# Optimization experiments

Hardware: AMD Instinct MI355X
Metric: run time of the kernel (lower is better)

Reference implementation:

```python
import jax, jax.numpy as jnp
import numpy as np

CODEBOOK_SIZE = 1024
EMBEDDING_DIM = 64


def setup_inputs() -> dict:
    key = jax.random.key(0)
    k_in, k_cb = jax.random.split(key)
    # latent feature (batch, embedding_dim, length)
    input = jax.random.normal(k_in, (16, EMBEDDING_DIM, 8192), dtype=jnp.float32)
    # learned codebook table (codebook_size, embedding_dim)
    codebook = jax.random.normal(k_cb, (CODEBOOK_SIZE, EMBEDDING_DIM), dtype=jnp.float32)
    return {"input": input, "codebook": codebook}


def reference(input, codebook):
    # input: (B, D, T); codebook: (K, D)
    B, D = input.shape[0], input.shape[1]
    spatial = input.shape[2:]
    # move embedding dim last and flatten tokens: (B*T, D)
    x = jnp.moveaxis(input, 1, -1).reshape(-1, D)
    x_sq = jnp.sum(x * x, axis=-1, keepdims=True)            # (N, 1)
    e_sq = jnp.sum(codebook * codebook, axis=-1)             # (K,)
    dist = x_sq - 2.0 * (x @ codebook.T) + e_sq[None, :]     # (N, K)
    indices = jnp.argmin(dist, axis=-1)                      # (N,)
    quantized = jnp.take(codebook, indices, axis=0)          # (N, D)
    # reshape back: output (B, D, *spatial), indices (B, *spatial)
    out = jnp.moveaxis(quantized.reshape((B,) + spatial + (D,)), -1, 1)
    idx = indices.reshape((B,) + spatial)
    return out, idx
```

## Files before the change

### kernel.cpp

```cpp
#include <hip/hip_runtime.h>
#include <float.h>

#define K_CODES 1024
#define DIM 64
#define T_LEN 8192
#define N_TOK 131072
#define LO_SCALE 2048.0f
#define LO_INV   (1.0f / 2048.0f)

typedef _Float16 half8 __attribute__((ext_vector_type(8)));
typedef float    f32x4 __attribute__((ext_vector_type(4)));

__global__ void vq_prep(const float* __restrict__ cb,
                        _Float16* __restrict__ whi,
                        _Float16* __restrict__ wlo,
                        float* __restrict__ wesq) {
    const int code = blockIdx.x * 256 + threadIdx.x;
    const float* row = cb + (size_t)code * DIM;
    float s = 0.0f;
    #pragma unroll
    for (int d0 = 0; d0 < DIM; d0 += 4) {
        float4 v = *reinterpret_cast<const float4*>(row + d0);
        float x[4] = {v.x, v.y, v.z, v.w};
        #pragma unroll
        for (int j = 0; j < 4; ++j) {
            float xx = x[j];
            _Float16 h = (_Float16)xx;
            _Float16 l = (_Float16)((xx - (float)h) * LO_SCALE);
            whi[(size_t)code * DIM + d0 + j] = h;
            wlo[(size_t)code * DIM + d0 + j] = l;
            s = fmaf(xx, xx, s);
        }
    }
    wesq[code] = s;
}

__global__ __launch_bounds__(256, 2)
void vq_main(const float* __restrict__ in,
             const float* __restrict__ cb,
             const _Float16* __restrict__ whi,
             const _Float16* __restrict__ wlo,
             const float* __restrict__ wesq,
             float* __restrict__ out) {
    __shared__ float esq_s[K_CODES];
    __shared__ int   idx_s[256];

    const int tid  = threadIdx.x;
    const int wave = tid >> 6;
    const int lane = tid & 63;
    const int lo4  = lane & 15;
    const int quad = lane >> 4;

    for (int k = tid; k < K_CODES; k += 256) esq_s[k] = wesq[k];
    __syncthreads();

    const int strip = (blockIdx.x * 4 + wave) * 64;
    const int b  = strip >> 13;
    const int t0 = strip & 8191;

    const float* xin = in + (size_t)b * DIM * T_LEN + t0;
    half8 a_hi[4][2], a_lo[4][2];
    #pragma unroll
    for (int mt = 0; mt < 4; ++mt) {
        #pragma unroll
        for (int s = 0; s < 2; ++s) {
            #pragma unroll
            for (int j = 0; j < 8; ++j) {
                const int d = s * 32 + quad * 8 + j;
                float x = xin[(size_t)d * T_LEN + mt * 16 + lo4];
                _Float16 h = (_Float16)x;
                _Float16 l = (_Float16)((x - (float)h) * LO_SCALE);
                a_hi[mt][s][j] = h;
                a_lo[mt][s][j] = l;
            }
        }
    }

    float best[16];
    int   bidx[16];
    #pragma unroll
    for (int i = 0; i < 16; ++i) { best[i] = FLT_MAX; bidx[i] = 0; }

    const _Float16* hbase = whi + (size_t)lo4 * DIM + quad * 8;
    const _Float16* lbase = wlo + (size_t)lo4 * DIM + quad * 8;

    half8 cbh0 = *(const half8*)(hbase);
    half8 cbh1 = *(const half8*)(hbase + 32);
    half8 cbl0 = *(const half8*)(lbase);
    half8 cbl1 = *(const half8*)(lbase + 32);
    float cesq = esq_s[lo4];

    for (int ct = 0; ct < 64; ++ct) {
        const int nct = (ct < 63) ? (ct + 1) : 63;
        const size_t noff = (size_t)nct * 16 * DIM;
        half8 nbh0 = *(const half8*)(hbase + noff);
        half8 nbh1 = *(const half8*)(hbase + noff + 32);
        half8 nbl0 = *(const half8*)(lbase + noff);
        half8 nbl1 = *(const half8*)(lbase + noff + 32);
        float nesq = esq_s[nct * 16 + lo4];

        const int code = ct * 16 + lo4;
        #pragma unroll
        for (int mt = 0; mt < 4; ++mt) {
            f32x4 acc1 = {0.f, 0.f, 0.f, 0.f};
            f32x4 acc2 = {0.f, 0.f, 0.f, 0.f};
            acc1 = __builtin_amdgcn_mfma_f32_16x16x32_f16(a_hi[mt][0], cbh0, acc1, 0, 0, 0);
            acc1 = __builtin_amdgcn_mfma_f32_16x16x32_f16(a_hi[mt][1], cbh1, acc1, 0, 0, 0);
            acc2 = __builtin_amdgcn_mfma_f32_16x16x32_f16(a_lo[mt][0], cbh0, acc2, 0, 0, 0);
            acc2 = __builtin_amdgcn_mfma_f32_16x16x32_f16(a_lo[mt][1], cbh1, acc2, 0, 0, 0);
            acc2 = __builtin_amdgcn_mfma_f32_16x16x32_f16(a_hi[mt][0], cbl0, acc2, 0, 0, 0);
            acc2 = __builtin_amdgcn_mfma_f32_16x16x32_f16(a_hi[mt][1], cbl1, acc2, 0, 0, 0);
            #pragma unroll
            for (int r = 0; r < 4; ++r) {
                float dot = fmaf(acc2[r], LO_INV, acc1[r]);
                float sc  = fmaf(dot, -2.0f, cesq);
                const int i = mt * 4 + r;
                bool lt = sc < best[i];
                best[i] = lt ? sc : best[i];
                bidx[i] = lt ? code : bidx[i];
            }
        }
        cbh0 = nbh0; cbh1 = nbh1; cbl0 = nbl0; cbl1 = nbl1; cesq = nesq;
    }

    #pragma unroll
    for (int i = 0; i < 16; ++i) {
        float s = best[i];
        int  ix = bidx[i];
        #pragma unroll
        for (int off = 1; off < 16; off <<= 1) {
            float s2 = __shfl_xor(s, off, 64);
            int  ix2 = __shfl_xor(ix, off, 64);
            bool take = (s2 < s) || (s2 == s && ix2 < ix);
            s  = take ? s2 : s;
            ix = take ? ix2 : ix;
        }
        if (lo4 == 0) {
            idx_s[wave * 64 + (i >> 2) * 16 + quad * 4 + (i & 3)] = ix;
        }
    }
    __syncthreads();

    const int my_idx = idx_s[wave * 64 + lane];
    out[(size_t)N_TOK * DIM + strip + lane] = (float)my_idx;

    const float* crow = cb + (size_t)my_idx * DIM;
    float* outv = out + (size_t)b * DIM * T_LEN + t0 + lane;
    #pragma unroll
    for (int d0 = 0; d0 < DIM; d0 += 4) {
        float4 v = *reinterpret_cast<const float4*>(crow + d0);
        outv[(size_t)(d0 + 0) * T_LEN] = v.x;
        outv[(size_t)(d0 + 1) * T_LEN] = v.y;
        outv[(size_t)(d0 + 2) * T_LEN] = v.z;
        outv[(size_t)(d0 + 3) * T_LEN] = v.w;
    }
}

extern "C" void kernel_launch(void* const* d_in, const int* in_sizes, int n_in,
                              void* d_out, int out_size, void* d_ws, size_t ws_size,
                              hipStream_t stream) {
    const float* in = (const float*)d_in[0];
    const float* cb = (const float*)d_in[1];
    float* out = (float*)d_out;

    _Float16* whi = (_Float16*)d_ws;
    _Float16* wlo = whi + (size_t)K_CODES * DIM;
    float*   wesq = (float*)(wlo + (size_t)K_CODES * DIM);

    vq_prep<<<dim3(K_CODES / 256), dim3(256), 0, stream>>>(cb, whi, wlo, wesq);
    vq_main<<<dim3(N_TOK / 256), dim3(256), 0, stream>>>(in, cb, whi, wlo, wesq, out);
}
```

Baseline: 153.8 us.

## Software-pipeline MFMA and argmin with double accumulators, fold scaling into inputs

The main loop is restructured into a ping-pong schedule: MFMAs for one code tile are issued while the argmin comparison runs on the previous tile's accumulators, so matrix-core latency is hidden behind VALU work. The -2 factor is folded into the fp16 input split and ||e||^2 seeds the hi accumulator, which removes one FMA per score. The prep kernel is also parallelised to 16 threads per code with vector stores and a shuffle reduction. The cost is more accumulator registers under the launch bound of two blocks, and a small rounding difference from scaling the inputs before the fp16 split.

```diff
diff --git a/kernel.cpp b/kernel.cpp
--- a/kernel.cpp
+++ b/kernel.cpp
@@ -9,30 +9,35 @@
 #define LO_INV   (1.0f / 2048.0f)
 
 typedef _Float16 half8 __attribute__((ext_vector_type(8)));
+typedef _Float16 half4 __attribute__((ext_vector_type(4)));
 typedef float    f32x4 __attribute__((ext_vector_type(4)));
 
 __global__ void vq_prep(const float* __restrict__ cb,
                         _Float16* __restrict__ whi,
                         _Float16* __restrict__ wlo,
                         float* __restrict__ wesq) {
-    const int code = blockIdx.x * 256 + threadIdx.x;
-    const float* row = cb + (size_t)code * DIM;
-    float s = 0.0f;
+    const int t = blockIdx.x * 256 + threadIdx.x;
+    const int code = t >> 4;
+    const int q    = t & 15;
+
+    float4 v = *reinterpret_cast<const float4*>(cb + (size_t)code * DIM + q * 4);
+    float x[4] = {v.x, v.y, v.z, v.w};
+    half4 h, l;
+    float psum = 0.0f;
     #pragma unroll
-    for (int d0 = 0; d0 < DIM; d0 += 4) {
-        float4 v = *reinterpret_cast<const float4*>(row + d0);
-        float x[4] = {v.x, v.y, v.z, v.w};
-        #pragma unroll
-        for (int j = 0; j < 4; ++j) {
-            float xx = x[j];
-            _Float16 h = (_Float16)xx;
-            _Float16 l = (_Float16)((xx - (float)h) * LO_SCALE);
-            whi[(size_t)code * DIM + d0 + j] = h;
-            wlo[(size_t)code * DIM + d0 + j] = l;
-            s = fmaf(xx, xx, s);
-        }
+    for (int j = 0; j < 4; ++j) {
+        _Float16 hh = (_Float16)x[j];
+        h[j] = hh;
+        l[j] = (_Float16)((x[j] - (float)hh) * LO_SCALE);
+        psum = fmaf(x[j], x[j], psum);
     }
-    wesq[code] = s;
+    *reinterpret_cast<half4*>(whi + (size_t)code * DIM + q * 4) = h;
+    *reinterpret_cast<half4*>(wlo + (size_t)code * DIM + q * 4) = l;
+
+    #pragma unroll
+    for (int off = 1; off < 16; off <<= 1)
+        psum += __shfl_xor(psum, off, 64);
+    if (q == 0) wesq[code] = psum;
 }
 
 __global__ __launch_bounds__(256, 2)
@@ -67,11 +72,10 @@
             #pragma unroll
             for (int j = 0; j < 8; ++j) {
                 const int d = s * 32 + quad * 8 + j;
-                float x = xin[(size_t)d * T_LEN + mt * 16 + lo4];
+                float x = -2.0f * xin[(size_t)d * T_LEN + mt * 16 + lo4];
                 _Float16 h = (_Float16)x;
-                _Float16 l = (_Float16)((x - (float)h) * LO_SCALE);
                 a_hi[mt][s][j] = h;
-                a_lo[mt][s][j] = l;
+                a_lo[mt][s][j] = (_Float16)((x - (float)h) * LO_SCALE);
             }
         }
     }
@@ -84,44 +88,63 @@
     const _Float16* hbase = whi + (size_t)lo4 * DIM + quad * 8;
     const _Float16* lbase = wlo + (size_t)lo4 * DIM + quad * 8;
 
-    half8 cbh0 = *(const half8*)(hbase);
-    half8 cbh1 = *(const half8*)(hbase + 32);
-    half8 cbl0 = *(const half8*)(lbase);
-    half8 cbl1 = *(const half8*)(lbase + 32);
-    float cesq = esq_s[lo4];
+    half8 beh0, beh1, bel0, bel1;
+    half8 boh0, boh1, bol0, bol1;
+    float ese, eso;
+    f32x4 accA1[4], accA2[4], accB1[4], accB2[4];
 
-    for (int ct = 0; ct < 64; ++ct) {
-        const int nct = (ct < 63) ? (ct + 1) : 63;
-        const size_t noff = (size_t)nct * 16 * DIM;
-        half8 nbh0 = *(const half8*)(hbase + noff);
-        half8 nbh1 = *(const half8*)(hbase + noff + 32);
-        half8 nbl0 = *(const half8*)(lbase + noff);
-        half8 nbl1 = *(const half8*)(lbase + noff + 32);
-        float nesq = esq_s[nct * 16 + lo4];
-
-        const int code = ct * 16 + lo4;
+    auto load_b = [&](int ct, half8& h0, half8& h1, half8& l0, half8& l1, float& es) {
+        const size_t off = (size_t)ct * 16 * DIM;
+        h0 = *(const half8*)(hbase + off);
+        h1 = *(const half8*)(hbase + off + 32);
+        l0 = *(const half8*)(lbase + off);
+        l1 = *(const half8*)(lbase + off + 32);
+        es = esq_s[ct * 16 + lo4];
+    };
+    auto mfma_step = [&](f32x4* a1, f32x4* a2, const half8& h0, const half8& h1,
+                         const half8& l0, const half8& l1, float cesq) {
         #pragma unroll
         for (int mt = 0; mt < 4; ++mt) {
-            f32x4 acc1 = {0.f, 0.f, 0.f, 0.f};
-            f32x4 acc2 = {0.f, 0.f, 0.f, 0.f};
-            acc1 = __builtin_amdgcn_mfma_f32_16x16x32_f16(a_hi[mt][0], cbh0, acc1, 0, 0, 0);
-            acc1 = __builtin_amdgcn_mfma_f32_16x16x32_f16(a_hi[mt][1], cbh1, acc1, 0, 0, 0);
-            acc2 = __builtin_amdgcn_mfma_f32_16x16x32_f16(a_lo[mt][0], cbh0, acc2, 0, 0, 0);
-            acc2 = __builtin_amdgcn_mfma_f32_16x16x32_f16(a_lo[mt][1], cbh1, acc2, 0, 0, 0);
-            acc2 = __builtin_amdgcn_mfma_f32_16x16x32_f16(a_hi[mt][0], cbl0, acc2, 0, 0, 0);
-            acc2 = __builtin_amdgcn_mfma_f32_16x16x32_f16(a_hi[mt][1], cbl1, acc2, 0, 0, 0);
+            f32x4 c1 = {cesq, cesq, cesq, cesq};
+            f32x4 c2 = {0.f, 0.f, 0.f, 0.f};
+            c1 = __builtin_amdgcn_mfma_f32_16x16x32_f16(a_hi[mt][0], h0, c1, 0, 0, 0);
+            c1 = __builtin_amdgcn_mfma_f32_16x16x32_f16(a_hi[mt][1], h1, c1, 0, 0, 0);
+            c2 = __builtin_amdgcn_mfma_f32_16x16x32_f16(a_lo[mt][0], h0, c2, 0, 0, 0);
+            c2 = __builtin_amdgcn_mfma_f32_16x16x32_f16(a_lo[mt][1], h1, c2, 0, 0, 0);
+            c2 = __builtin_amdgcn_mfma_f32_16x16x32_f16(a_hi[mt][0], l0, c2, 0, 0, 0);
+            c2 = __builtin_amdgcn_mfma_f32_16x16x32_f16(a_hi[mt][1], l1, c2, 0, 0, 0);
+            a1[mt] = c1;
+            a2[mt] = c2;
+        }
+    };
+    auto argmin_step = [&](const f32x4* a1, const f32x4* a2, int code) {
+        #pragma unroll
+        for (int mt = 0; mt < 4; ++mt) {
             #pragma unroll
             for (int r = 0; r < 4; ++r) {
-                float dot = fmaf(acc2[r], LO_INV, acc1[r]);
-                float sc  = fmaf(dot, -2.0f, cesq);
+                float sc = fmaf(a2[mt][r], LO_INV, a1[mt][r]);
                 const int i = mt * 4 + r;
                 bool lt = sc < best[i];
                 best[i] = lt ? sc : best[i];
                 bidx[i] = lt ? code : bidx[i];
             }
         }
-        cbh0 = nbh0; cbh1 = nbh1; cbl0 = nbl0; cbl1 = nbl1; cesq = nesq;
+    };
+
+    load_b(0, beh0, beh1, bel0, bel1, ese);
+    load_b(1, boh0, boh1, bol0, bol1, eso);
+    mfma_step(accA1, accA2, beh0, beh1, bel0, bel1, ese);
+    for (int p = 1; p <= 31; ++p) {
+        load_b(2 * p, beh0, beh1, bel0, bel1, ese);
+        mfma_step(accB1, accB2, boh0, boh1, bol0, bol1, eso);
+        argmin_step(accA1, accA2, (2 * p - 2) * 16 + lo4);
+        load_b(2 * p + 1, boh0, boh1, bol0, bol1, eso);
+        mfma_step(accA1, accA2, beh0, beh1, bel0, bel1, ese);
+        argmin_step(accB1, accB2, (2 * p - 1) * 16 + lo4);
     }
+    mfma_step(accB1, accB2, boh0, boh1, bol0, bol1, eso);
+    argmin_step(accA1, accA2, 62 * 16 + lo4);
+    argmin_step(accB1, accB2, 63 * 16 + lo4);
 
     #pragma unroll
     for (int i = 0; i < 16; ++i) {
@@ -167,6 +190,6 @@
     _Float16* wlo = whi + (size_t)K_CODES * DIM;
     float*   wesq = (float*)(wlo + (size_t)K_CODES * DIM);
 
-    vq_prep<<<dim3(K_CODES / 256), dim3(256), 0, stream>>>(cb, whi, wlo, wesq);
+    vq_prep<<<dim3(K_CODES * 16 / 256), dim3(256), 0, stream>>>(cb, whi, wlo, wesq);
     vq_main<<<dim3(N_TOK / 256), dim3(256), 0, stream>>>(in, cb, whi, wlo, wesq, out);
 }
```

Result: faster. 149.9 us (-2.6%).

## Fuse codebook prep into main VQ kernel with on-the-fly split and fp32 loads

Applied to the files above, without the earlier changes.

Removes the separate codebook preprocessing kernel. Each wave now loads the fp32 codebook directly, computes the squared norms with shuffles, and splits each value into hi/lo fp16 halves inline. The -2 factor is folded into the input and the norm is used as the MFMA accumulator seed, which drops the per-score fma. Waves handle 32 tokens instead of 64 to raise occupancy (launch bounds 4), and the gather/writeback is spread over all 256 threads. In exchange, every wave redoes the codebook conversion and norm work, software prefetch of the next tile is gone, and the hi/lo split of the codebook now uses truncation plus round-toward-zero conversion, which could change tie behaviour.

```diff
diff --git a/kernel.cpp b/kernel.cpp
--- a/kernel.cpp
+++ b/kernel.cpp
@@ -8,42 +8,26 @@
 #define LO_SCALE 2048.0f
 #define LO_INV   (1.0f / 2048.0f)
 
-typedef _Float16 half8 __attribute__((ext_vector_type(8)));
-typedef float    f32x4 __attribute__((ext_vector_type(4)));
+typedef _Float16 half8  __attribute__((ext_vector_type(8)));
+typedef _Float16 half2v __attribute__((ext_vector_type(2)));
+typedef __fp16   fp16x2 __attribute__((ext_vector_type(2)));
+typedef float    f32x4  __attribute__((ext_vector_type(4)));
 
-__global__ void vq_prep(const float* __restrict__ cb,
-                        _Float16* __restrict__ whi,
-                        _Float16* __restrict__ wlo,
-                        float* __restrict__ wesq) {
-    const int code = blockIdx.x * 256 + threadIdx.x;
-    const float* row = cb + (size_t)code * DIM;
-    float s = 0.0f;
-    #pragma unroll
-    for (int d0 = 0; d0 < DIM; d0 += 4) {
-        float4 v = *reinterpret_cast<const float4*>(row + d0);
-        float x[4] = {v.x, v.y, v.z, v.w};
-        #pragma unroll
-        for (int j = 0; j < 4; ++j) {
-            float xx = x[j];
-            _Float16 h = (_Float16)xx;
-            _Float16 l = (_Float16)((xx - (float)h) * LO_SCALE);
-            whi[(size_t)code * DIM + d0 + j] = h;
-            wlo[(size_t)code * DIM + d0 + j] = l;
-            s = fmaf(xx, xx, s);
-        }
-    }
-    wesq[code] = s;
+union H8 { half8 v; half2v p[4]; };
+
+__device__ inline void split2(float x0, float x1, half2v& h, half2v& l) {
+    float h0 = __uint_as_float(__float_as_uint(x0) & 0xFFFFE000u);
+    float h1 = __uint_as_float(__float_as_uint(x1) & 0xFFFFE000u);
+    h = __builtin_bit_cast(half2v, __builtin_amdgcn_cvt_pkrtz(h0, h1));
+    l = __builtin_bit_cast(half2v, __builtin_amdgcn_cvt_pkrtz((x0 - h0) * LO_SCALE,
+                                                              (x1 - h1) * LO_SCALE));
 }
 
-__global__ __launch_bounds__(256, 2)
-void vq_main(const float* __restrict__ in,
-             const float* __restrict__ cb,
-             const _Float16* __restrict__ whi,
-             const _Float16* __restrict__ wlo,
-             const float* __restrict__ wesq,
-             float* __restrict__ out) {
-    __shared__ float esq_s[K_CODES];
-    __shared__ int   idx_s[256];
+__global__ __launch_bounds__(256, 4)
+void vq_fused(const float* __restrict__ in,
+              const float* __restrict__ cb,
+              float* __restrict__ out) {
+    __shared__ int idx_s[128];
 
     const int tid  = threadIdx.x;
     const int wave = tid >> 6;
@@ -51,80 +35,90 @@
     const int lo4  = lane & 15;
     const int quad = lane >> 4;
 
-    for (int k = tid; k < K_CODES; k += 256) esq_s[k] = wesq[k];
-    __syncthreads();
-
-    const int strip = (blockIdx.x * 4 + wave) * 64;
+    const int strip = blockIdx.x * 128 + wave * 32;
     const int b  = strip >> 13;
     const int t0 = strip & 8191;
 
     const float* xin = in + (size_t)b * DIM * T_LEN + t0;
-    half8 a_hi[4][2], a_lo[4][2];
+    half8 a_hi[2][2], a_lo[2][2];
     #pragma unroll
-    for (int mt = 0; mt < 4; ++mt) {
+    for (int mt = 0; mt < 2; ++mt) {
         #pragma unroll
         for (int s = 0; s < 2; ++s) {
+            H8 hh, ll;
             #pragma unroll
-            for (int j = 0; j < 8; ++j) {
-                const int d = s * 32 + quad * 8 + j;
-                float x = xin[(size_t)d * T_LEN + mt * 16 + lo4];
-                _Float16 h = (_Float16)x;
-                _Float16 l = (_Float16)((x - (float)h) * LO_SCALE);
-                a_hi[mt][s][j] = h;
-                a_lo[mt][s][j] = l;
+            for (int jp = 0; jp < 4; ++jp) {
+                const int d0 = s * 32 + quad * 8 + jp * 2;
+                float x0 = -2.0f * xin[(size_t)(d0 + 0) * T_LEN + mt * 16 + lo4];
+                float x1 = -2.0f * xin[(size_t)(d0 + 1) * T_LEN + mt * 16 + lo4];
+                _Float16 h0 = (_Float16)x0, h1 = (_Float16)x1;
+                half2v hp, lp;
+                hp[0] = h0; hp[1] = h1;
+                lp[0] = (_Float16)((x0 - (float)h0) * LO_SCALE);
+                lp[1] = (_Float16)((x1 - (float)h1) * LO_SCALE);
+                hh.p[jp] = hp; ll.p[jp] = lp;
             }
+            a_hi[mt][s] = hh.v;
+            a_lo[mt][s] = ll.v;
         }
     }
 
-    float best[16];
-    int   bidx[16];
+    float best[8];
+    int   bidx[8];
     #pragma unroll
-    for (int i = 0; i < 16; ++i) { best[i] = FLT_MAX; bidx[i] = 0; }
+    for (int i = 0; i < 8; ++i) { best[i] = FLT_MAX; bidx[i] = 0; }
 
-    const _Float16* hbase = whi + (size_t)lo4 * DIM + quad * 8;
-    const _Float16* lbase = wlo + (size_t)lo4 * DIM + quad * 8;
-
-    half8 cbh0 = *(const half8*)(hbase);
-    half8 cbh1 = *(const half8*)(hbase + 32);
-    half8 cbl0 = *(const half8*)(lbase);
-    half8 cbl1 = *(const half8*)(lbase + 32);
-    float cesq = esq_s[lo4];
+    const float* bbase = cb + (size_t)lo4 * DIM + quad * 8;
 
     for (int ct = 0; ct < 64; ++ct) {
-        const int nct = (ct < 63) ? (ct + 1) : 63;
-        const size_t noff = (size_t)nct * 16 * DIM;
-        half8 nbh0 = *(const half8*)(hbase + noff);
-        half8 nbh1 = *(const half8*)(hbase + noff + 32);
-        half8 nbl0 = *(const half8*)(lbase + noff);
-        half8 nbl1 = *(const half8*)(lbase + noff + 32);
-        float nesq = esq_s[nct * 16 + lo4];
+        const float* bp = bbase + (size_t)ct * 16 * DIM;
+        float4 f0 = *reinterpret_cast<const float4*>(bp);
+        float4 f1 = *reinterpret_cast<const float4*>(bp + 4);
+        float4 f2 = *reinterpret_cast<const float4*>(bp + 32);
+        float4 f3 = *reinterpret_cast<const float4*>(bp + 36);
+
+        float p0 = fmaf(f0.x, f0.x, fmaf(f0.y, f0.y, fmaf(f0.z, f0.z, f0.w * f0.w)));
+        float p1 = fmaf(f1.x, f1.x, fmaf(f1.y, f1.y, fmaf(f1.z, f1.z, f1.w * f1.w)));
+        float p2 = fmaf(f2.x, f2.x, fmaf(f2.y, f2.y, fmaf(f2.z, f2.z, f2.w * f2.w)));
+        float p3 = fmaf(f3.x, f3.x, fmaf(f3.y, f3.y, fmaf(f3.z, f3.z, f3.w * f3.w)));
+        float pe = (p0 + p1) + (p2 + p3);
+        pe += __shfl_xor(pe, 16, 64);
+        pe += __shfl_xor(pe, 32, 64);
+
+        H8 bh0, bl0, bh1, bl1;
+        split2(f0.x, f0.y, bh0.p[0], bl0.p[0]);
+        split2(f0.z, f0.w, bh0.p[1], bl0.p[1]);
+        split2(f1.x, f1.y, bh0.p[2], bl0.p[2]);
+        split2(f1.z, f1.w, bh0.p[3], bl0.p[3]);
+        split2(f2.x, f2.y, bh1.p[0], bl1.p[0]);
+        split2(f2.z, f2.w, bh1.p[1], bl1.p[1]);
+        split2(f3.x, f3.y, bh1.p[2], bl1.p[2]);
+        split2(f3.z, f3.w, bh1.p[3], bl1.p[3]);
 
         const int code = ct * 16 + lo4;
         #pragma unroll
-        for (int mt = 0; mt < 4; ++mt) {
-            f32x4 acc1 = {0.f, 0.f, 0.f, 0.f};
-            f32x4 acc2 = {0.f, 0.f, 0.f, 0.f};
-            acc1 = __builtin_amdgcn_mfma_f32_16x16x32_f16(a_hi[mt][0], cbh0, acc1, 0, 0, 0);
-            acc1 = __builtin_amdgcn_mfma_f32_16x16x32_f16(a_hi[mt][1], cbh1, acc1, 0, 0, 0);
-            acc2 = __builtin_amdgcn_mfma_f32_16x16x32_f16(a_lo[mt][0], cbh0, acc2, 0, 0, 0);
-            acc2 = __builtin_amdgcn_mfma_f32_16x16x32_f16(a_lo[mt][1], cbh1, acc2, 0, 0, 0);
-            acc2 = __builtin_amdgcn_mfma_f32_16x16x32_f16(a_hi[mt][0], cbl0, acc2, 0, 0, 0);
-            acc2 = __builtin_amdgcn_mfma_f32_16x16x32_f16(a_hi[mt][1], cbl1, acc2, 0, 0, 0);
+        for (int mt = 0; mt < 2; ++mt) {
+            f32x4 c1 = {pe, pe, pe, pe};
+            f32x4 c2 = {0.f, 0.f, 0.f, 0.f};
+            c1 = __builtin_amdgcn_mfma_f32_16x16x32_f16(a_hi[mt][0], bh0.v, c1, 0, 0, 0);
+            c1 = __builtin_amdgcn_mfma_f32_16x16x32_f16(a_hi[mt][1], bh1.v, c1, 0, 0, 0);
+            c2 = __builtin_amdgcn_mfma_f32_16x16x32_f16(a_lo[mt][0], bh0.v, c2, 0, 0, 0);
+            c2 = __builtin_amdgcn_mfma_f32_16x16x32_f16(a_lo[mt][1], bh1.v, c2, 0, 0, 0);
+            c2 = __builtin_amdgcn_mfma_f32_16x16x32_f16(a_hi[mt][0], bl0.v, c2, 0, 0, 0);
+            c2 = __builtin_amdgcn_mfma_f32_16x16x32_f16(a_hi[mt][1], bl1.v, c2, 0, 0, 0);
             #pragma unroll
             for (int r = 0; r < 4; ++r) {
-                float dot = fmaf(acc2[r], LO_INV, acc1[r]);
-                float sc  = fmaf(dot, -2.0f, cesq);
+                float sc = fmaf(c2[r], LO_INV, c1[r]);
                 const int i = mt * 4 + r;
                 bool lt = sc < best[i];
                 best[i] = lt ? sc : best[i];
                 bidx[i] = lt ? code : bidx[i];
             }
         }
-        cbh0 = nbh0; cbh1 = nbh1; cbl0 = nbl0; cbl1 = nbl1; cesq = nesq;
     }
 
     #pragma unroll
-    for (int i = 0; i < 16; ++i) {
+    for (int i = 0; i < 8; ++i) {
         float s = best[i];
         int  ix = bidx[i];
         #pragma unroll
@@ -136,18 +130,25 @@
             ix = take ? ix2 : ix;
         }
         if (lo4 == 0) {
-            idx_s[wave * 64 + (i >> 2) * 16 + quad * 4 + (i & 3)] = ix;
+            idx_s[wave * 32 + (i >> 2) * 16 + quad * 4 + (i & 3)] = ix;
         }
     }
     __syncthreads();
 
-    const int my_idx = idx_s[wave * 64 + lane];
-    out[(size_t)N_TOK * DIM + strip + lane] = (float)my_idx;
+    const int tok_local = tid & 127;
+    const int dhalf = tid >> 7;
+    const int token = blockIdx.x * 128 + tok_local;
+    const int tb = token >> 13;
+    const int tt = token & 8191;
+    const int my_idx = idx_s[tok_local];
 
-    const float* crow = cb + (size_t)my_idx * DIM;
-    float* outv = out + (size_t)b * DIM * T_LEN + t0 + lane;
+    if (dhalf == 0)
+        out[(size_t)N_TOK * DIM + token] = (float)my_idx;
+
+    const float* crow = cb + (size_t)my_idx * DIM + dhalf * 32;
+    float* outv = out + (size_t)tb * DIM * T_LEN + (size_t)(dhalf * 32) * T_LEN + tt;
     #pragma unroll
-    for (int d0 = 0; d0 < DIM; d0 += 4) {
+    for (int d0 = 0; d0 < 32; d0 += 4) {
         float4 v = *reinterpret_cast<const float4*>(crow + d0);
         outv[(size_t)(d0 + 0) * T_LEN] = v.x;
         outv[(size_t)(d0 + 1) * T_LEN] = v.y;
@@ -163,10 +164,5 @@
     const float* cb = (const float*)d_in[1];
     float* out = (float*)d_out;
 
-    _Float16* whi = (_Float16*)d_ws;
-    _Float16* wlo = whi + (size_t)K_CODES * DIM;
-    float*   wesq = (float*)(wlo + (size_t)K_CODES * DIM);
-
-    vq_prep<<<dim3(K_CODES / 256), dim3(256), 0, stream>>>(cb, whi, wlo, wesq);
-    vq_main<<<dim3(N_TOK / 256), dim3(256), 0, stream>>>(in, cb, whi, wlo, wesq, out);
+    vq_fused<<<dim3(N_TOK / 128), dim3(256), 0, stream>>>(in, cb, out);
 }
```

New measurement: 197.8 us. 1.29x slower.
